# Kernel tuning notes

Hardware: AMD Instinct MI355X
Metric: run time of the kernel (lower is better)

## Reference

```python
import jax, jax.numpy as jnp
import numpy as np

N = 50000      # nodes
E = 500000     # edges
D = 128        # in_dim == out_dim
L = 4          # encoder_layers
G = 64         # graphs in batch
FIXED = 10000  # fixed_input_dim
BN_EPS = 1e-5


def setup_inputs() -> dict:
    key = jax.random.key(0)
    ks = jax.random.split(key, 14)
    s = 0.05
    feat_id = jax.random.randint(ks[0], (N,), 0, FIXED)
    edge_index = jax.random.randint(ks[1], (2, E), 0, N)
    # sorted graph assignment guaranteeing all G graphs are non-empty
    batch = (jnp.arange(N) * G) // N
    return {
        "feat_id": feat_id,
        "edge_index": edge_index,
        "batch": batch,
        # value_projection: Linear(FIXED, D); store weight.T as a lookup table
        "value_proj_w": jax.random.normal(ks[2], (FIXED, D)) * s,
        "value_proj_b": jax.random.normal(ks[3], (D,)) * s,
        "deg_emb": jax.random.normal(ks[4], (1001, D)) * s,
        # stacked per-layer GIN MLP params: Linear -> BN -> ReLU -> Linear
        "mlp_w1": jax.random.normal(ks[5], (L, D, D)) * s,
        "mlp_b1": jax.random.normal(ks[6], (L, D)) * s,
        "bn1_g": 1.0 + 0.1 * jax.random.normal(ks[7], (L, D)),
        "bn1_b": 0.1 * jax.random.normal(ks[8], (L, D)),
        "mlp_w2": jax.random.normal(ks[9], (L, D, D)) * s,
        "mlp_b2": jax.random.normal(ks[10], (L, D)) * s,
        # outer per-layer BatchNorm1d
        "bn2_g": 1.0 + 0.1 * jax.random.normal(ks[11], (L, D)),
        "bn2_b": 0.1 * jax.random.normal(ks[12], (L, D)),
    }


def _bn(x, g, b):
    # BatchNorm1d in training mode: batch stats over the node axis, biased var
    mu = jnp.mean(x, axis=0)
    var = jnp.mean(jnp.square(x - mu), axis=0)
    return g * (x - mu) * jax.lax.rsqrt(var + BN_EPS) + b


def reference(feat_id, edge_index, batch, value_proj_w, value_proj_b, deg_emb,
              mlp_w1, mlp_b1, bn1_g, bn1_b, mlp_w2, mlp_b2, bn2_g, bn2_b):
    src, dst = edge_index[0], edge_index[1]
    # one_hot(feat_id % FIXED) @ W.T + b  ==  gather of transposed weight rows
    h_attr = value_proj_w[feat_id % FIXED] + value_proj_b  # [N, D]
    # in-degree embedding (clamped to [0, 1000])
    in_deg = jax.ops.segment_sum(jnp.ones((E,), jnp.int32), dst, num_segments=N)
    h = h_attr + deg_emb[jnp.clip(in_deg, 0, 1000)]
    for i in range(L):
        # GIN: sum_{j in N(v)} h_j + (1 + eps) * h_v, eps = 0 (learn_eps=False)
        agg = jax.ops.segment_sum(h[src], dst, num_segments=N) + h
        z = jax.nn.relu(_bn(agg @ mlp_w1[i] + mlp_b1[i], bn1_g[i], bn1_b[i]))
        z = z @ mlp_w2[i] + mlp_b2[i]
        h = jax.nn.relu(_bn(z, bn2_g[i], bn2_b[i]))
    # global mean pool per graph
    gsum = jax.ops.segment_sum(h, batch, num_segments=G)       # [G, D]
    cnt = jax.ops.segment_sum(jnp.ones((N, 1)), batch, num_segments=G)
    graph_feature = gsum / jnp.maximum(cnt, 1.0)
    return graph_feature, h
```

## Files before the change

### kernel.cpp

```cpp
#include <hip/hip_runtime.h>

#define NN 50000
#define NE 500000
#define DD 128
#define NL 4
#define NG 64
#define FIXED_DIM 10000
#define BN_EPS 1e-5f
#define NB 196

typedef unsigned short u16;
typedef unsigned int u32;
typedef __attribute__((ext_vector_type(8))) short bf16x8;
typedef __attribute__((ext_vector_type(4))) float f32x4;

__device__ __forceinline__ float bf2f(u16 u) {
    return __uint_as_float(((u32)u) << 16);
}
__device__ __forceinline__ u16 f2bf(float f) {
    u32 u = __float_as_uint(f);
    return (u16)((u + 0x7FFFu + ((u >> 16) & 1u)) >> 16);
}
__device__ __forceinline__ float ldf(const void* p, size_t i, int isbf) {
    return isbf ? bf2f(((const u16*)p)[i]) : ((const float*)p)[i];
}

__global__ void k_pre(const void* __restrict__ vb, int* __restrict__ flag,
                      const int* __restrict__ batch, int* __restrict__ goff,
                      float* __restrict__ zbase, int zwords) {
    int b = blockIdx.x, t = threadIdx.x;
    if (b == 0) {
        __shared__ int ok[256];
        float v = (t < 128) ? bf2f(((const u16*)vb)[t]) : 0.f;
        ok[t] = (t < 128) ? ((fabsf(v) < 1000.f) ? 1 : 0) : 1;
        __syncthreads();
        for (int off = 128; off; off >>= 1) {
            if (t < off) ok[t] &= ok[t + off];
            __syncthreads();
        }
        if (t == 0) *flag = ok[0];
    } else if (b == 1) {
        if (t <= NG) {
            int lo = 0, hi = NN;
            while (lo < hi) {
                int mid = (lo + hi) >> 1;
                if (batch[mid] < t) lo = mid + 1; else hi = mid;
            }
            goff[t] = lo;
        }
    } else {
        int i = (b - 2) * 256 + t;
        if (i < zwords) zbase[i] = 0.f;
    }
}

__global__ void k_cvt6(const void* b1, const void* b2, const void* g1,
                       const void* be1, const void* g2, const void* be2,
                       float* __restrict__ pc, const int* __restrict__ flag) {
    int t = blockIdx.x * 256 + threadIdx.x;
    if (t >= 6 * NL * DD) return;
    int p = t >> 9, j = t & 511;
    const void* s = (p == 0) ? b1 : (p == 1) ? b2 : (p == 2) ? g1
                  : (p == 3) ? be1 : (p == 4) ? g2 : be2;
    pc[t] = ldf(s, j, *flag);
}
__global__ void k_deg(const int* __restrict__ dst, int* __restrict__ deg) {
    int i = blockIdx.x * 256 + threadIdx.x;
    if (i < NE) atomicAdd(&deg[dst[i]], 1);
}

__global__ void k_scan1(const int* __restrict__ deg, int* __restrict__ bsum) {
    __shared__ int S[256];
    int b = blockIdx.x, t = threadIdx.x;
    int i = b * 256 + t;
    S[t] = (i < NN) ? deg[i] : 0;
    __syncthreads();
    for (int off = 128; off; off >>= 1) {
        if (t < off) S[t] += S[t + off];
        __syncthreads();
    }
    if (t == 0) bsum[b] = S[0];
}
__global__ void k_scan2(int* __restrict__ bsum) {
    __shared__ int S[256];
    int t = threadIdx.x;
    int v = (t < NB) ? bsum[t] : 0;
    S[t] = v;
    __syncthreads();
    for (int off = 1; off < 256; off <<= 1) {
        int x = (t >= off) ? S[t - off] : 0;
        __syncthreads();
        S[t] += x;
        __syncthreads();
    }
    if (t < NB) bsum[t] = S[t] - v;
}
__global__ void k_scan3(const int* __restrict__ deg, const int* __restrict__ bsum,
                        int* __restrict__ rowptr) {
    __shared__ int S[256];
    int b = blockIdx.x, t = threadIdx.x;
    int i = b * 256 + t;
    int v = (i < NN) ? deg[i] : 0;
    S[t] = v;
    __syncthreads();
    for (int off = 1; off < 256; off <<= 1) {
        int x = (t >= off) ? S[t - off] : 0;
        __syncthreads();
        S[t] += x;
        __syncthreads();
    }
    if (i < NN) rowptr[i] = bsum[b] + S[t] - v;
    if (i == NN - 1) rowptr[NN] = bsum[b] + S[t];
}

__global__ void k_fill(const int* __restrict__ src, const int* __restrict__ dst,
                       const int* __restrict__ rowptr, int* __restrict__ cursor,
                       int* __restrict__ colidx) {
    int e = blockIdx.x * 256 + threadIdx.x;
    if (e >= NE) return;
    int d = dst[e];
    int p = atomicAdd(&cursor[d], 1);
    colidx[rowptr[d] + p] = src[e];
}

__global__ void k_swz(const void* __restrict__ w1, const void* __restrict__ w2,
                      u16* __restrict__ Wsw, const int* __restrict__ flag) {
    int t = blockIdx.x * 256 + threadIdx.x;
    if (t >= 8 * 16384) return;
    int m    = t >> 14;
    int idx  = t & 16383;
    int nt   = idx >> 11;
    int ks   = (idx >> 9) & 3;
    int lane = (idx >> 3) & 63;
    int j    = idx & 7;
    int row = ks * 32 + (lane >> 4) * 8 + j;
    int col = nt * 16 + (lane & 15);
    const void* src = (m < 4) ? w1 : w2;
    size_t off = (size_t)(m & 3) * DD * DD + (size_t)row * DD + col;
    Wsw[t] = f2bf(ldf(src, off, *flag));
}

__global__ void k_init(const int* __restrict__ feat, const int* __restrict__ deg,
                       const void* __restrict__ vw, const void* __restrict__ vb,
                       const void* __restrict__ demb, u16* __restrict__ B,
                       const int* __restrict__ flag) {
    int t = blockIdx.x * 256 + threadIdx.x;
    if (t >= NN * DD) return;
    int n = t >> 7, c = t & 127;
    int isbf = *flag;
    int f = feat[n] % FIXED_DIM;
    int dg = min(deg[n], 1000);
    B[t] = f2bf(ldf(vw, (size_t)f * DD + c, isbf)
              + ldf(vb, c, isbf)
              + ldf(demb, (size_t)dg * DD + c, isbf));
}

template <bool AFF>
__global__ __launch_bounds__(256, 8) void k_aggr(
        const u16* __restrict__ B, const int* __restrict__ rowptr,
        const int* __restrict__ colidx,
        const float* __restrict__ gIn, const float* __restrict__ bIn,
        const float* __restrict__ sIn, const float* __restrict__ qIn,
        u16* __restrict__ Agg) {
    int n = blockIdx.x * 4 + (threadIdx.x >> 6);
    if (n >= NN) return;
    int c = (threadIdx.x & 63) * 2;
    float a0 = 1.f, b0 = 0.f, a1 = 1.f, b1 = 0.f;
    if (AFF) {
        float inv = 1.0f / (float)NN;
        float mu0 = sIn[c] * inv, mu1 = sIn[c + 1] * inv;
        float v0 = fmaxf(qIn[c] * inv - mu0 * mu0, 0.f);
        float v1 = fmaxf(qIn[c + 1] * inv - mu1 * mu1, 0.f);
        a0 = gIn[c] * rsqrtf(v0 + BN_EPS);
        a1 = gIn[c + 1] * rsqrtf(v1 + BN_EPS);
        b0 = bIn[c] - a0 * mu0;
        b1 = bIn[c + 1] - a1 * mu1;
    }
    u32 w = *(const u32*)&B[(size_t)n * DD + c];
    float x0 = bf2f((u16)(w & 0xFFFF)), x1 = bf2f((u16)(w >> 16));
    float s0 = AFF ? fmaxf(fmaf(a0, x0, b0), 0.f) : x0;
    float s1 = AFF ? fmaxf(fmaf(a1, x1, b1), 0.f) : x1;
    int lo = rowptr[n], hi = rowptr[n + 1];
    int j = lo;
    for (; j + 4 <= hi; j += 4) {
        int m0 = colidx[j], m1 = colidx[j + 1];
        int m2 = colidx[j + 2], m3 = colidx[j + 3];
        u32 w0 = *(const u32*)&B[(size_t)m0 * DD + c];
        u32 w1v = *(const u32*)&B[(size_t)m1 * DD + c];
        u32 w2v = *(const u32*)&B[(size_t)m2 * DD + c];
        u32 w3v = *(const u32*)&B[(size_t)m3 * DD + c];
        float y;
        y = bf2f((u16)(w0 & 0xFFFF)); s0 += AFF ? fmaxf(fmaf(a0, y, b0), 0.f) : y;
        y = bf2f((u16)(w0 >> 16));    s1 += AFF ? fmaxf(fmaf(a1, y, b1), 0.f) : y;
        y = bf2f((u16)(w1v & 0xFFFF)); s0 += AFF ? fmaxf(fmaf(a0, y, b0), 0.f) : y;
        y = bf2f((u16)(w1v >> 16));    s1 += AFF ? fmaxf(fmaf(a1, y, b1), 0.f) : y;
        y = bf2f((u16)(w2v & 0xFFFF)); s0 += AFF ? fmaxf(fmaf(a0, y, b0), 0.f) : y;
        y = bf2f((u16)(w2v >> 16));    s1 += AFF ? fmaxf(fmaf(a1, y, b1), 0.f) : y;
        y = bf2f((u16)(w3v & 0xFFFF)); s0 += AFF ? fmaxf(fmaf(a0, y, b0), 0.f) : y;
        y = bf2f((u16)(w3v >> 16));    s1 += AFF ? fmaxf(fmaf(a1, y, b1), 0.f) : y;
    }
    for (; j < hi; j++) {
        int m = colidx[j];
        w = *(const u32*)&B[(size_t)m * DD + c];
        x0 = bf2f((u16)(w & 0xFFFF)); x1 = bf2f((u16)(w >> 16));
        s0 += AFF ? fmaxf(fmaf(a0, x0, b0), 0.f) : x0;
        s1 += AFF ? fmaxf(fmaf(a1, x1, b1), 0.f) : x1;
    }
    *(u32*)&Agg[(size_t)n * DD + c] = ((u32)f2bf(s1) << 16) | (u32)f2bf(s0);
}

template <bool IN16, bool OUT16, bool AFF>
__global__ __launch_bounds__(256, 2) void k_gemm(
        const void* In, const u16* __restrict__ Wsw,
        const float* __restrict__ bias,
        const float* __restrict__ gIn, const float* __restrict__ bIn,
        const float* __restrict__ sIn, const float* __restrict__ qIn,
        void* Out, float* __restrict__ ssum, float* __restrict__ ssq,
        int nRows) {
    __shared__ u16 Wl[16384];
    __shared__ u16 At[128 * 136];
    __shared__ float affS[256];
    float* RedS = (float*)At;
    float* RedQ = RedS + 512;
    const int t = threadIdx.x;
    const int row0 = blockIdx.x * 128;

    if (AFF) {
        if (t < 128) {
            float inv = 1.0f / (float)NN;
            float mu = sIn[t] * inv;
            float var = fmaxf(qIn[t] * inv - mu * mu, 0.f);
            float a = gIn[t] * rsqrtf(var + BN_EPS);
            affS[t] = a;
            affS[128 + t] = bIn[t] - a * mu;
        }
        __syncthreads();
    }

    {
        const uint4* s = (const uint4*)Wsw;
        uint4* d = (uint4*)Wl;
        #pragma unroll
        for (int i = 0; i < 8; i++) d[t + i * 256] = s[t + i * 256];
    }
    if (IN16) {
        for (int i = t; i < 2048; i += 256) {
            int r  = i >> 4;
            int c8 = (i & 15) * 8;
            int gr = row0 + r;
            uint4 v = make_uint4(0u, 0u, 0u, 0u);
            if (gr < nRows) v = *(const uint4*)&((const u16*)In)[(size_t)gr * DD + c8];
            *(uint4*)&At[r * 136 + c8] = v;
        }
    } else {
        for (int i = t; i < 4096; i += 256) {
            int r  = i >> 5;
            int c4 = (i & 31) * 4;
            int gr = row0 + r;
            float4 v = make_float4(0.f, 0.f, 0.f, 0.f);
            if (gr < nRows) {
                v = *(const float4*)&((const float*)In)[(size_t)gr * DD + c4];
                if (AFF) {
                    v.x = fmaxf(fmaf(affS[c4 + 0], v.x, affS[128 + c4 + 0]), 0.f);
                    v.y = fmaxf(fmaf(affS[c4 + 1], v.y, affS[128 + c4 + 1]), 0.f);
                    v.z = fmaxf(fmaf(affS[c4 + 2], v.z, affS[128 + c4 + 2]), 0.f);
                    v.w = fmaxf(fmaf(affS[c4 + 3], v.w, affS[128 + c4 + 3]), 0.f);
                }
            }
            ushort4 o;
            o.x = f2bf(v.x); o.y = f2bf(v.y); o.z = f2bf(v.z); o.w = f2bf(v.w);
            *(ushort4*)&At[r * 136 + c4] = o;
        }
    }
    __syncthreads();

    const int w    = t >> 6;
    const int ln   = t & 63;
    const int quad = ln >> 4;
    const int lq   = ln & 15;

    f32x4 acc0[8], acc1[8];
    #pragma unroll
    for (int nt = 0; nt < 8; nt++) {
        acc0[nt] = (f32x4){0.f, 0.f, 0.f, 0.f};
        acc1[nt] = (f32x4){0.f, 0.f, 0.f, 0.f};
    }

    const u16* aRow0 = &At[(w * 32 + lq) * 136 + quad * 8];
    const u16* aRow1 = &At[(w * 32 + 16 + lq) * 136 + quad * 8];
    #pragma unroll
    for (int ks = 0; ks < 4; ks++) {
        bf16x8 a0 = *(const bf16x8*)&aRow0[ks * 32];
        bf16x8 a1 = *(const bf16x8*)&aRow1[ks * 32];
        #pragma unroll
        for (int nt = 0; nt < 8; nt++) {
            bf16x8 b = *(const bf16x8*)&Wl[((nt * 4 + ks) * 64 + ln) * 8];
            acc0[nt] = __builtin_amdgcn_mfma_f32_16x16x32_bf16(a0, b, acc0[nt], 0, 0, 0);
            acc1[nt] = __builtin_amdgcn_mfma_f32_16x16x32_bf16(a1, b, acc1[nt], 0, 0, 0);
        }
    }
    __syncthreads();

    const int rb0 = row0 + w * 32 + quad * 4;
    const int rb1 = rb0 + 16;
    #pragma unroll
    for (int nt = 0; nt < 8; nt++) {
        int col = nt * 16 + lq;
        float bv = bias[col];
        float s = 0.f, q = 0.f;
        #pragma unroll
        for (int r = 0; r < 4; r++) {
            int gr = rb0 + r;
            if (gr < nRows) {
                float val = acc0[nt][r] + bv;
                size_t o = (size_t)gr * DD + col;
                if (OUT16) ((u16*)Out)[o] = f2bf(val);
                else       ((float*)Out)[o] = val;
                s += val; q += val * val;
            }
        }
        #pragma unroll
        for (int r = 0; r < 4; r++) {
            int gr = rb1 + r;
            if (gr < nRows) {
                float val = acc1[nt][r] + bv;
                size_t o = (size_t)gr * DD + col;
                if (OUT16) ((u16*)Out)[o] = f2bf(val);
                else       ((float*)Out)[o] = val;
                s += val; q += val * val;
            }
        }
        s += __shfl_xor(s, 16); q += __shfl_xor(q, 16);
        s += __shfl_xor(s, 32); q += __shfl_xor(q, 32);
        if (quad == 0) { RedS[w * 128 + col] = s; RedQ[w * 128 + col] = q; }
    }
    __syncthreads();
    if (t < 128) {
        float s = RedS[t] + RedS[128 + t] + RedS[256 + t] + RedS[384 + t];
        float q = RedQ[t] + RedQ[128 + t] + RedQ[256 + t] + RedQ[384 + t];
        atomicAdd(&ssum[t], s);
        atomicAdd(&ssq[t], q);
    }
}

__global__ __launch_bounds__(256, 4) void k_update2(
        const u16* __restrict__ Bz,
        const float* __restrict__ gIn, const float* __restrict__ bIn,
        const float* __restrict__ sIn, const float* __restrict__ qIn,
        const int* __restrict__ batch, float* __restrict__ A,
        float* __restrict__ gsum) {
    const int t = threadIdx.x;
    const int c = t & 127;
    const int half = t >> 7;
    const int r0 = blockIdx.x * 64;
    float inv = 1.0f / (float)NN;
    float mu = sIn[c] * inv;
    float var = fmaxf(qIn[c] * inv - mu * mu, 0.f);
    float a = gIn[c] * rsqrtf(var + BN_EPS);
    float bb = bIn[c] - a * mu;
    float acc = 0.f;
    int curg = -1;
    for (int i = 0; i < 32; i++) {
        int r = r0 + half + 2 * i;
        if (r >= NN) break;
        int gg = batch[r];
        if (gg != curg) {
            if (curg >= 0) atomicAdd(&gsum[(size_t)curg * DD + c], acc);
            acc = 0.f; curg = gg;
        }
        float v = fmaxf(fmaf(a, bf2f(Bz[(size_t)r * DD + c]), bb), 0.f);
        A[(size_t)r * DD + c] = v;
        acc += v;
    }
    if (curg >= 0) atomicAdd(&gsum[(size_t)curg * DD + c], acc);
}

__global__ void k_pool2(const float* __restrict__ gsum, const int* __restrict__ goff,
                        float* __restrict__ out) {
    int t = blockIdx.x * 256 + threadIdx.x;
    int g = t >> 7;
    float cnt = fmaxf((float)(goff[g + 1] - goff[g]), 1.0f);
    out[t] = gsum[t] / cnt;
}

extern "C" void kernel_launch(void* const* d_in, const int* in_sizes, int n_in,
                              void* d_out, int out_size, void* d_ws, size_t ws_size,
                              hipStream_t stream) {
    const int* feat  = (const int*)d_in[0];
    const int* ei    = (const int*)d_in[1];
    const int* batch = (const int*)d_in[2];
    const void* vw   = d_in[3];
    const void* vb   = d_in[4];
    const void* demb = d_in[5];
    const void* w1   = d_in[6];
    const void* b1   = d_in[7];
    const void* g1   = d_in[8];
    const void* be1  = d_in[9];
    const void* w2   = d_in[10];
    const void* b2   = d_in[11];
    const void* g2   = d_in[12];
    const void* be2  = d_in[13];

    const int* src = ei;
    const int* dst = ei + NE;
    const size_t ND = (size_t)NN * DD;

    float* pc     = (float*)d_ws;
    int*   flag   = (int*)(pc + 3072);
    float* stats  = (float*)(flag + 64);
    float* gsum   = stats + 2048;
    int*   deg    = (int*)(gsum + 8192);
    int*   cursor = deg + NN;
    int*   bsum   = cursor + NN;
    int*   goff   = bsum + 256;
    int*   rowptr = goff + 128;
    int*   colidx = rowptr + NN + 64;
    u16*   Wsw    = (u16*)(colidx + NE);
    u16*   B      = Wsw + 8 * 16384;
    u16*   Agg16  = B + ND;

    float* b1c  = pc;
    float* b2c  = pc + 512;
    float* g1c  = pc + 1024;
    float* be1c = pc + 1536;
    float* g2c  = pc + 2048;
    float* be2c = pc + 2560;
    float* sum1 = stats;
    float* sq1  = stats + 512;
    float* sum2 = stats + 1024;
    float* sq2  = stats + 1536;

    float* outw = (float*)d_out;
    float* A    = outw + (size_t)NG * DD;

    const int zwords = 2048 + 8192 + NN + NN;
    const int gridND = (int)((ND + 255) / 256);
    const int gemmBlocks = (NN + 127) / 128;
    const int aggrBlocks = (NN + 3) / 4;

    k_pre<<<2 + (zwords + 255) / 256, 256, 0, stream>>>(vb, flag, batch, goff,
                                                        stats, zwords);
    k_cvt6<<<(6 * NL * DD + 255) / 256, 256, 0, stream>>>(b1, b2, g1, be1, g2, be2, pc, flag);
    k_swz<<<(8 * 16384) / 256, 256, 0, stream>>>(w1, w2, Wsw, flag);
    k_deg<<<(NE + 255) / 256, 256, 0, stream>>>(dst, deg);
    k_scan1<<<NB, 256, 0, stream>>>(deg, bsum);
    k_scan2<<<1, 256, 0, stream>>>(bsum);
    k_scan3<<<NB, 256, 0, stream>>>(deg, bsum, rowptr);
    k_fill<<<(NE + 255) / 256, 256, 0, stream>>>(src, dst, rowptr, cursor, colidx);
    k_init<<<gridND, 256, 0, stream>>>(feat, deg, vw, vb, demb, B, flag);

    for (int l = 0; l < NL; l++) {
        const u16* W1l = Wsw + (size_t)l * 16384;
        const u16* W2l = Wsw + (size_t)(4 + l) * 16384;
        if (l == 0) {
            k_aggr<false><<<aggrBlocks, 256, 0, stream>>>(
                B, rowptr, colidx, nullptr, nullptr, nullptr, nullptr, Agg16);
        } else {
            k_aggr<true><<<aggrBlocks, 256, 0, stream>>>(
                B, rowptr, colidx, g2c + (l - 1) * 128, be2c + (l - 1) * 128,
                sum2 + (l - 1) * 128, sq2 + (l - 1) * 128, Agg16);
        }
        k_gemm<true, false, false><<<gemmBlocks, 256, 0, stream>>>(
            Agg16, W1l, b1c + l * 128, nullptr, nullptr, nullptr, nullptr,
            A, sum1 + l * 128, sq1 + l * 128, NN);
        k_gemm<false, true, true><<<gemmBlocks, 256, 0, stream>>>(
            A, W2l, b2c + l * 128, g1c + l * 128, be1c + l * 128,
            sum1 + l * 128, sq1 + l * 128,
            B, sum2 + l * 128, sq2 + l * 128, NN);
    }
    k_update2<<<(NN + 63) / 64, 256, 0, stream>>>(
        B, g2c + 3 * 128, be2c + 3 * 128, sum2 + 3 * 128, sq2 + 3 * 128,
        batch, A, gsum);
    k_pool2<<<(NG * DD + 255) / 256, 256, 0, stream>>>(gsum, goff, outw);
}
```

Before: 527.7 us.

## Merge setup kernels with last-block semaphores and halve GEMM row tile

Fuses the parameter conversion and weight swizzle into one launch. Fuses scan1 and scan2 through a last-block atomic semaphore, scan3 with the node init, and the final update with pooling, again via a last-block semaphore. Together these cut the kernel launch count and its fixed overhead. Separately, the GEMM tile drops from 128 to 64 rows per block with a higher occupancy bound, giving more blocks and lower LDS and register use, but each block now loads the full weight matrix for half as many rows.

After: 643.5 us. 22.0% more time.

```diff
diff --git a/kernel.cpp b/kernel.cpp
--- a/kernel.cpp
+++ b/kernel.cpp
@@ -54,23 +54,43 @@
     }
 }
 
-__global__ void k_cvt6(const void* b1, const void* b2, const void* g1,
-                       const void* be1, const void* g2, const void* be2,
-                       float* __restrict__ pc, const int* __restrict__ flag) {
-    int t = blockIdx.x * 256 + threadIdx.x;
-    if (t >= 6 * NL * DD) return;
-    int p = t >> 9, j = t & 511;
-    const void* s = (p == 0) ? b1 : (p == 1) ? b2 : (p == 2) ? g1
-                  : (p == 3) ? be1 : (p == 4) ? g2 : be2;
-    pc[t] = ldf(s, j, *flag);
-}
+__global__ void k_cvtswz(const void* b1, const void* b2, const void* g1,
+                         const void* be1, const void* g2, const void* be2,
+                         const void* __restrict__ w1, const void* __restrict__ w2,
+                         float* __restrict__ pc, u16* __restrict__ Wsw,
+                         const int* __restrict__ flag) {
+    int b = blockIdx.x, tt = threadIdx.x;
+    if (b < 12) {
+        int t = b * 256 + tt;
+        int p = t >> 9, j = t & 511;
+        const void* s = (p == 0) ? b1 : (p == 1) ? b2 : (p == 2) ? g1
+                      : (p == 3) ? be1 : (p == 4) ? g2 : be2;
+        pc[t] = ldf(s, j, *flag);
+    } else {
+        int t = (b - 12) * 256 + tt;
+        int m    = t >> 14;
+        int idx  = t & 16383;
+        int nt   = idx >> 11;
+        int ks   = (idx >> 9) & 3;
+        int lane = (idx >> 3) & 63;
+        int j    = idx & 7;
+        int row = ks * 32 + (lane >> 4) * 8 + j;
+        int col = nt * 16 + (lane & 15);
+        const void* src = (m < 4) ? w1 : w2;
+        size_t off = (size_t)(m & 3) * DD * DD + (size_t)row * DD + col;
+        Wsw[t] = f2bf(ldf(src, off, *flag));
+    }
+}
+
 __global__ void k_deg(const int* __restrict__ dst, int* __restrict__ deg) {
     int i = blockIdx.x * 256 + threadIdx.x;
     if (i < NE) atomicAdd(&deg[dst[i]], 1);
 }
 
-__global__ void k_scan1(const int* __restrict__ deg, int* __restrict__ bsum) {
+__global__ void k_scan12(const int* __restrict__ deg, int* __restrict__ bsum,
+                         int* __restrict__ sem) {
     __shared__ int S[256];
+    __shared__ int lastB;
     int b = blockIdx.x, t = threadIdx.x;
     int i = b * 256 + t;
     S[t] = (i < NN) ? deg[i] : 0;
@@ -79,12 +99,15 @@
         if (t < off) S[t] += S[t + off];
         __syncthreads();
     }
-    if (t == 0) bsum[b] = S[0];
-}
-__global__ void k_scan2(int* __restrict__ bsum) {
-    __shared__ int S[256];
-    int t = threadIdx.x;
-    int v = (t < NB) ? bsum[t] : 0;
+    if (t == 0) {
+        atomicExch(&bsum[b], S[0]);
+        __threadfence();
+        lastB = (atomicAdd(&sem[0], 1) == gridDim.x - 1);
+    }
+    __syncthreads();
+    if (!lastB) return;
+    __threadfence();
+    int v = (t < NB) ? atomicAdd(&bsum[t], 0) : 0;
     S[t] = v;
     __syncthreads();
     for (int off = 1; off < 256; off <<= 1) {
@@ -95,22 +118,38 @@
     }
     if (t < NB) bsum[t] = S[t] - v;
 }
-__global__ void k_scan3(const int* __restrict__ deg, const int* __restrict__ bsum,
-                        int* __restrict__ rowptr) {
+
+__global__ void k_scan3init(const int* __restrict__ deg, const int* __restrict__ bsum,
+                            int* __restrict__ rowptr,
+                            const int* __restrict__ feat, const void* __restrict__ vw,
+                            const void* __restrict__ vb, const void* __restrict__ demb,
+                            u16* __restrict__ B, const int* __restrict__ flag) {
     __shared__ int S[256];
     int b = blockIdx.x, t = threadIdx.x;
-    int i = b * 256 + t;
-    int v = (i < NN) ? deg[i] : 0;
-    S[t] = v;
-    __syncthreads();
-    for (int off = 1; off < 256; off <<= 1) {
-        int x = (t >= off) ? S[t - off] : 0;
-        __syncthreads();
-        S[t] += x;
-        __syncthreads();
-    }
-    if (i < NN) rowptr[i] = bsum[b] + S[t] - v;
-    if (i == NN - 1) rowptr[NN] = bsum[b] + S[t];
+    if (b < NB) {
+        int i = b * 256 + t;
+        int v = (i < NN) ? deg[i] : 0;
+        S[t] = v;
+        __syncthreads();
+        for (int off = 1; off < 256; off <<= 1) {
+            int x = (t >= off) ? S[t - off] : 0;
+            __syncthreads();
+            S[t] += x;
+            __syncthreads();
+        }
+        if (i < NN) rowptr[i] = bsum[b] + S[t] - v;
+        if (i == NN - 1) rowptr[NN] = bsum[b] + S[t];
+    } else {
+        int idx = (b - NB) * 256 + t;
+        if (idx >= NN * DD) return;
+        int n = idx >> 7, c = idx & 127;
+        int isbf = *flag;
+        int f = feat[n] % FIXED_DIM;
+        int dg = min(deg[n], 1000);
+        B[idx] = f2bf(ldf(vw, (size_t)f * DD + c, isbf)
+                    + ldf(vb, c, isbf)
+                    + ldf(demb, (size_t)dg * DD + c, isbf));
+    }
 }
 
 __global__ void k_fill(const int* __restrict__ src, const int* __restrict__ dst,
@@ -121,38 +160,6 @@
     int d = dst[e];
     int p = atomicAdd(&cursor[d], 1);
     colidx[rowptr[d] + p] = src[e];
-}
-
-__global__ void k_swz(const void* __restrict__ w1, const void* __restrict__ w2,
-                      u16* __restrict__ Wsw, const int* __restrict__ flag) {
-    int t = blockIdx.x * 256 + threadIdx.x;
-    if (t >= 8 * 16384) return;
-    int m    = t >> 14;
-    int idx  = t & 16383;
-    int nt   = idx >> 11;
-    int ks   = (idx >> 9) & 3;
-    int lane = (idx >> 3) & 63;
-    int j    = idx & 7;
-    int row = ks * 32 + (lane >> 4) * 8 + j;
-    int col = nt * 16 + (lane & 15);
-    const void* src = (m < 4) ? w1 : w2;
-    size_t off = (size_t)(m & 3) * DD * DD + (size_t)row * DD + col;
-    Wsw[t] = f2bf(ldf(src, off, *flag));
-}
-
-__global__ void k_init(const int* __restrict__ feat, const int* __restrict__ deg,
-                       const void* __restrict__ vw, const void* __restrict__ vb,
-                       const void* __restrict__ demb, u16* __restrict__ B,
-                       const int* __restrict__ flag) {
-    int t = blockIdx.x * 256 + threadIdx.x;
-    if (t >= NN * DD) return;
-    int n = t >> 7, c = t & 127;
-    int isbf = *flag;
-    int f = feat[n] % FIXED_DIM;
-    int dg = min(deg[n], 1000);
-    B[t] = f2bf(ldf(vw, (size_t)f * DD + c, isbf)
-              + ldf(vb, c, isbf)
-              + ldf(demb, (size_t)dg * DD + c, isbf));
 }
 
 template <bool AFF>
@@ -210,7 +217,7 @@
 }
 
 template <bool IN16, bool OUT16, bool AFF>
-__global__ __launch_bounds__(256, 2) void k_gemm(
+__global__ __launch_bounds__(256, 3) void k_gemm(
         const void* In, const u16* __restrict__ Wsw,
         const float* __restrict__ bias,
         const float* __restrict__ gIn, const float* __restrict__ bIn,
@@ -218,12 +225,12 @@
         void* Out, float* __restrict__ ssum, float* __restrict__ ssq,
         int nRows) {
     __shared__ u16 Wl[16384];
-    __shared__ u16 At[128 * 136];
+    __shared__ u16 At[64 * 136];
     __shared__ float affS[256];
     float* RedS = (float*)At;
     float* RedQ = RedS + 512;
     const int t = threadIdx.x;
-    const int row0 = blockIdx.x * 128;
+    const int row0 = blockIdx.x * 64;
 
     if (AFF) {
         if (t < 128) {
@@ -244,7 +251,8 @@
         for (int i = 0; i < 8; i++) d[t + i * 256] = s[t + i * 256];
     }
     if (IN16) {
-        for (int i = t; i < 2048; i += 256) {
+        #pragma unroll
+        for (int i = t; i < 1024; i += 256) {
             int r  = i >> 4;
             int c8 = (i & 15) * 8;
             int gr = row0 + r;
@@ -253,7 +261,8 @@
             *(uint4*)&At[r * 136 + c8] = v;
         }
     } else {
-        for (int i = t; i < 4096; i += 256) {
+        #pragma unroll
+        for (int i = t; i < 2048; i += 256) {
             int r  = i >> 5;
             int c4 = (i & 31) * 4;
             int gr = row0 + r;
@@ -279,30 +288,23 @@
     const int quad = ln >> 4;
     const int lq   = ln & 15;
 
-    f32x4 acc0[8], acc1[8];
+    f32x4 acc[8];
     #pragma unroll
-    for (int nt = 0; nt < 8; nt++) {
-        acc0[nt] = (f32x4){0.f, 0.f, 0.f, 0.f};
-        acc1[nt] = (f32x4){0.f, 0.f, 0.f, 0.f};
-    }
-
-    const u16* aRow0 = &At[(w * 32 + lq) * 136 + quad * 8];
-    const u16* aRow1 = &At[(w * 32 + 16 + lq) * 136 + quad * 8];
+    for (int nt = 0; nt < 8; nt++) acc[nt] = (f32x4){0.f, 0.f, 0.f, 0.f};
+
+    const u16* aRow = &At[(w * 16 + lq) * 136 + quad * 8];
     #pragma unroll
     for (int ks = 0; ks < 4; ks++) {
-        bf16x8 a0 = *(const bf16x8*)&aRow0[ks * 32];
-        bf16x8 a1 = *(const bf16x8*)&aRow1[ks * 32];
+        bf16x8 a = *(const bf16x8*)&aRow[ks * 32];
         #pragma unroll
         for (int nt = 0; nt < 8; nt++) {
             bf16x8 b = *(const bf16x8*)&Wl[((nt * 4 + ks) * 64 + ln) * 8];
-            acc0[nt] = __builtin_amdgcn_mfma_f32_16x16x32_bf16(a0, b, acc0[nt], 0, 0, 0);
-            acc1[nt] = __builtin_amdgcn_mfma_f32_16x16x32_bf16(a1, b, acc1[nt], 0, 0, 0);
-        }
-    }
-    __syncthreads();
-
-    const int rb0 = row0 + w * 32 + quad * 4;
-    const int rb1 = rb0 + 16;
+            acc[nt] = __builtin_amdgcn_mfma_f32_16x16x32_bf16(a, b, acc[nt], 0, 0, 0);
+        }
+    }
+    __syncthreads();
+
+    const int rb = row0 + w * 16 + quad * 4;
     #pragma unroll
     for (int nt = 0; nt < 8; nt++) {
         int col = nt * 16 + lq;
@@ -310,26 +312,15 @@
         float s = 0.f, q = 0.f;
         #pragma unroll
         for (int r = 0; r < 4; r++) {
-            int gr = rb0 + r;
+            int gr = rb + r;
             if (gr < nRows) {
-                float val = acc0[nt][r] + bv;
+                float val = acc[nt][r] + bv;
                 size_t o = (size_t)gr * DD + col;
                 if (OUT16) ((u16*)Out)[o] = f2bf(val);
                 else       ((float*)Out)[o] = val;
                 s += val; q += val * val;
             }
         }
-        #pragma unroll
-        for (int r = 0; r < 4; r++) {
-            int gr = rb1 + r;
-            if (gr < nRows) {
-                float val = acc1[nt][r] + bv;
-                size_t o = (size_t)gr * DD + col;
-                if (OUT16) ((u16*)Out)[o] = f2bf(val);
-                else       ((float*)Out)[o] = val;
-                s += val; q += val * val;
-            }
-        }
         s += __shfl_xor(s, 16); q += __shfl_xor(q, 16);
         s += __shfl_xor(s, 32); q += __shfl_xor(q, 32);
         if (quad == 0) { RedS[w * 128 + col] = s; RedQ[w * 128 + col] = q; }
@@ -343,12 +334,13 @@
     }
 }
 
-__global__ __launch_bounds__(256, 4) void k_update2(
+__global__ __launch_bounds__(256, 4) void k_upool(
         const u16* __restrict__ Bz,
         const float* __restrict__ gIn, const float* __restrict__ bIn,
         const float* __restrict__ sIn, const float* __restrict__ qIn,
         const int* __restrict__ batch, float* __restrict__ A,
-        float* __restrict__ gsum) {
+        float* __restrict__ gsum, const int* __restrict__ goff,
+        float* __restrict__ outw, int* __restrict__ sem) {
     const int t = threadIdx.x;
     const int c = t & 127;
     const int half = t >> 7;
@@ -373,14 +365,20 @@
         acc += v;
     }
     if (curg >= 0) atomicAdd(&gsum[(size_t)curg * DD + c], acc);
-}
-
-__global__ void k_pool2(const float* __restrict__ gsum, const int* __restrict__ goff,
-                        float* __restrict__ out) {
-    int t = blockIdx.x * 256 + threadIdx.x;
-    int g = t >> 7;
-    float cnt = fmaxf((float)(goff[g + 1] - goff[g]), 1.0f);
-    out[t] = gsum[t] / cnt;
+
+    __shared__ int lastF;
+    if (t == 0) {
+        __threadfence();
+        lastF = (atomicAdd(&sem[1], 1) == gridDim.x - 1);
+    }
+    __syncthreads();
+    if (!lastF) return;
+    __threadfence();
+    for (int i = t; i < NG * DD; i += 256) {
+        int g = i >> 7;
+        float cnt = fmaxf((float)(goff[g + 1] - goff[g]), 1.0f);
+        outw[i] = atomicAdd(&gsum[i], 0.0f) / cnt;
+    }
 }
 
 extern "C" void kernel_launch(void* const* d_in, const int* in_sizes, int n_in,
@@ -411,7 +409,8 @@
     float* gsum   = stats + 2048;
     int*   deg    = (int*)(gsum + 8192);
     int*   cursor = deg + NN;
-    int*   bsum   = cursor + NN;
+    int*   sem    = cursor + NN;
+    int*   bsum   = sem + 64;
     int*   goff   = bsum + 256;
     int*   rowptr = goff + 128;
     int*   colidx = rowptr + NN + 64;
@@ -433,21 +432,20 @@
     float* outw = (float*)d_out;
     float* A    = outw + (size_t)NG * DD;
 
-    const int zwords = 2048 + 8192 + NN + NN;
-    const int gridND = (int)((ND + 255) / 256);
-    const int gemmBlocks = (NN + 127) / 128;
+    const int zwords = 2048 + 8192 + NN + NN + 64;
+    const int gridND = (int)(ND / 256);
+    const int gemmBlocks = (NN + 63) / 64;
     const int aggrBlocks = (NN + 3) / 4;
 
     k_pre<<<2 + (zwords + 255) / 256, 256, 0, stream>>>(vb, flag, batch, goff,
                                                         stats, zwords);
-    k_cvt6<<<(6 * NL * DD + 255) / 256, 256, 0, stream>>>(b1, b2, g1, be1, g2, be2, pc, flag);
-    k_swz<<<(8 * 16384) / 256, 256, 0, stream>>>(w1, w2, Wsw, flag);
+    k_cvtswz<<<12 + 512, 256, 0, stream>>>(b1, b2, g1, be1, g2, be2, w1, w2,
+                                           pc, Wsw, flag);
     k_deg<<<(NE + 255) / 256, 256, 0, stream>>>(dst, deg);
-    k_scan1<<<NB, 256, 0, stream>>>(deg, bsum);
-    k_scan2<<<1, 256, 0, stream>>>(bsum);
-    k_scan3<<<NB, 256, 0, stream>>>(deg, bsum, rowptr);
+    k_scan12<<<NB, 256, 0, stream>>>(deg, bsum, sem);
+    k_scan3init<<<NB + gridND, 256, 0, stream>>>(deg, bsum, rowptr,
+                                                 feat, vw, vb, demb, B, flag);
     k_fill<<<(NE + 255) / 256, 256, 0, stream>>>(src, dst, rowptr, cursor, colidx);
-    k_init<<<gridND, 256, 0, stream>>>(feat, deg, vw, vb, demb, B, flag);
 
     for (int l = 0; l < NL; l++) {
         const u16* W1l = Wsw + (size_t)l * 16384;
@@ -468,8 +466,7 @@
             sum1 + l * 128, sq1 + l * 128,
             B, sum2 + l * 128, sq2 + l * 128, NN);
     }
-    k_update2<<<(NN + 63) / 64, 256, 0, stream>>>(
+    k_upool<<<(NN + 63) / 64, 256, 0, stream>>>(
         B, g2c + 3 * 128, be2c + 3 * 128, sum2 + 3 * 128, sq2 + 3 * 128,
-        batch, A, gsum);
-    k_pool2<<<(NG * DD + 255) / 256, 256, 0, stream>>>(gsum, goff, outw);
-}
+        batch, A, gsum, goff, outw, sem);
+}
```
